# Kernel tuning notes

Hardware: AMD Instinct MI355X
Metric: run time of the kernel (lower is better)

## Reference

```python
import jax, jax.numpy as jnp
import numpy as np

B, C, L = 32, 512, 4096
H, K = 8, 3            # heads, kernel_size
D = C // H             # head dim
G = 32                 # GroupNorm groups
PAD = (K - 1) // 2
EPS = 1e-5
NEG = -1e30


def setup_inputs() -> dict:
    key = jax.random.key(0)
    ks = jax.random.split(key, 7)
    s = 0.02
    return {
        "x": jax.random.normal(ks[0], (B, C, L), dtype=jnp.float32),
        "gamma": jnp.ones((C,), dtype=jnp.float32),
        "beta": jnp.zeros((C,), dtype=jnp.float32),
        "W_k": jax.random.normal(ks[1], (C, H * D), dtype=jnp.float32) * s,
        "W_v": jax.random.normal(ks[2], (C, H * D), dtype=jnp.float32) * s,
        "W_o": jax.random.normal(ks[3], (H * D, C), dtype=jnp.float32) * s,
        "q": jax.random.normal(ks[4], (H, D), dtype=jnp.float32) * s,     # learned queries (QnA)
        "rpe": jax.random.normal(ks[5], (H, K), dtype=jnp.float32) * s,   # relative-position bias
    }


def _group_norm(x, gamma, beta):
    # x: (B, C, L); normalize over (C//G, L) within each of G groups
    b, c, l = x.shape
    xg = x.reshape(b, G, (c // G) * l)
    mu = jnp.mean(xg, axis=-1, keepdims=True)
    var = jnp.var(xg, axis=-1, keepdims=True)
    xn = ((xg - mu) * jax.lax.rsqrt(var + EPS)).reshape(b, c, l)
    return xn * gamma[None, :, None] + beta[None, :, None]


def reference(x, gamma, beta, W_k, W_v, W_o, q, rpe):
    h = _group_norm(x, gamma, beta)                     # (B, C, L)
    ht = jnp.transpose(h, (0, 2, 1))                    # (B, L, C)
    k = (ht @ W_k).reshape(B, L, H, D)                  # (B, L, H, D)
    v = (ht @ W_v).reshape(B, L, H, D)

    scale = 1.0 / np.sqrt(D).astype(np.float32)
    logits = jnp.einsum('blhd,hd->blh', k, q) * scale   # (B, L, H)

    # sliding windows of size K (zero-padded; -inf logits at boundaries)
    lp = jnp.pad(logits, ((0, 0), (PAD, PAD), (0, 0)), constant_values=NEG)
    lwin = jnp.stack([lp[:, j:j + L] for j in range(K)], axis=2)      # (B, L, K, H)
    lwin = lwin + jnp.transpose(rpe)[None, None]                       # rpe: (H,K)->(K,H)
    attn = jax.nn.softmax(lwin, axis=2)                                # (B, L, K, H)

    vp = jnp.pad(v, ((0, 0), (PAD, PAD), (0, 0), (0, 0)))
    vwin = jnp.stack([vp[:, j:j + L] for j in range(K)], axis=2)       # (B, L, K, H, D)
    o = jnp.einsum('blkh,blkhd->blhd', attn, vwin).reshape(B, L, H * D)

    out = (o @ W_o)                                      # (B, L, C)
    return x + jnp.transpose(out, (0, 2, 1))             # residual, (B, C, L)
```

## Files before the change

### kernel.cpp

```cpp
#include <hip/hip_runtime.h>

#define Bb 32
#define Cc 512
#define Ll 4096
#define Hh 8
#define Dd 64
#define Gg 32
#define BLt (Bb * Ll)
#define NKV 520
#define NKVPAD 640

typedef __attribute__((ext_vector_type(4))) float f32x4;
typedef __attribute__((ext_vector_type(8))) short short8;
typedef __attribute__((ext_vector_type(4))) short s16x4;
typedef __attribute__((ext_vector_type(4))) int int4v;

union U16 { int4v v; short s[8]; };

__device__ __forceinline__ float bf2f(short s) {
    unsigned u = ((unsigned)(unsigned short)s) << 16;
    float f; __builtin_memcpy(&f, &u, 4); return f;
}
__device__ __forceinline__ short f2bf(float f) {
    unsigned u; __builtin_memcpy(&u, &f, 4);
    u = (u + 0x7FFFu + ((u >> 16) & 1u)) >> 16;
    return (short)u;
}

__device__ __forceinline__ int kpack(int k) {
    int blk = k >> 5, r = k & 31;
    return blk * 32 + ((r & 15) >> 2) * 8 + ((r >> 4) << 2) + (r & 3);
}

__device__ __forceinline__ int swz_off(int row, int inner) {
    return row * 128 + (inner ^ ((row & 7) << 4));
}

__device__ __forceinline__ void gload16(const short* g, short* l) {
    __builtin_amdgcn_global_load_lds((const __attribute__((address_space(1))) unsigned int*)g,
                                     (__attribute__((address_space(3))) unsigned int*)l,
                                     16, 0, 0);
}

__global__ void k_prep(const float* __restrict__ Wk, const float* __restrict__ Wv,
                       const float* __restrict__ Wo, const float* __restrict__ q,
                       short* __restrict__ Wct, short* __restrict__ Wot, int packWo)
{
    int bid = blockIdx.x, t = threadIdx.x;
    if (bid < NKVPAD) {
        int n = bid;
        if (n < 512) {
            for (int k = t; k < 512; k += 64)
                Wct[n * 512 + kpack(k)] = f2bf(Wv[k * 512 + n]);
        } else if (n < NKV) {
            int h = n - 512;
            for (int k = t; k < 512; k += 64) {
                float acc = 0.f;
                for (int d = 0; d < 64; ++d)
                    acc += Wk[k * 512 + h * 64 + d] * q[h * 64 + d];
                Wct[n * 512 + kpack(k)] = f2bf(acc * 0.125f);
            }
        } else {
            for (int k = t; k < 512; k += 64) Wct[n * 512 + kpack(k)] = 0;
        }
    } else {
        int c = bid - NKVPAD;
        for (int k = t; k < 512; k += 64)
            Wot[c * 512 + (packWo ? kpack(k) : k)] = f2bf(Wo[k * 512 + c]);
    }
}

__global__ void k_stats(const float* __restrict__ x, float* __restrict__ stats)
{
    int bg = blockIdx.x;
    const float* p = x + (size_t)bg * 65536;
    int t = threadIdx.x;
    float s = 0.f, ss = 0.f;
    for (int i = t * 4; i < 65536; i += 1024) {
        f32x4 v = *(const f32x4*)(p + i);
        s  += v[0] + v[1] + v[2] + v[3];
        ss += v[0]*v[0] + v[1]*v[1] + v[2]*v[2] + v[3]*v[3];
    }
    for (int o = 32; o > 0; o >>= 1) { s += __shfl_down(s, o); ss += __shfl_down(ss, o); }
    __shared__ float red[8];
    int lane = t & 63, w = t >> 6;
    if (lane == 0) { red[w] = s; red[4 + w] = ss; }
    __syncthreads();
    if (t == 0) {
        float S  = red[0] + red[1] + red[2] + red[3];
        float SS = red[4] + red[5] + red[6] + red[7];
        float mean = S * (1.0f / 65536.0f);
        float var  = SS * (1.0f / 65536.0f) - mean * mean;
        stats[bg * 2]     = mean;
        stats[bg * 2 + 1] = rsqrtf(var + 1e-5f);
    }
}

__global__ void k_norm_t(const float* __restrict__ x, const float* __restrict__ gamma,
                         const float* __restrict__ beta, const float* __restrict__ stats,
                         short* __restrict__ hT)
{
    __shared__ float tile[64 * 65];
    int b = blockIdx.z, c0 = blockIdx.y * 64, l0 = blockIdx.x * 64;
    int t = threadIdx.x;
    int lq = t & 15, cq = t >> 4;
    #pragma unroll
    for (int p = 0; p < 4; ++p) {
        int cl = cq + p * 16;
        int c = c0 + cl;
        float mean = stats[(b * 32 + (c >> 4)) * 2];
        float rstd = stats[(b * 32 + (c >> 4)) * 2 + 1];
        float a  = rstd * gamma[c];
        float bb = beta[c] - mean * a;
        f32x4 v = *(const f32x4*)(x + ((size_t)b << 21) + ((size_t)c << 12) + l0 + lq * 4);
        #pragma unroll
        for (int j = 0; j < 4; ++j) tile[cl * 65 + lq * 4 + j] = v[j] * a + bb;
    }
    __syncthreads();
    int ll = t >> 2, cq4 = t & 3;
    int bl = b * Ll + l0 + ll;
    short hbuf[16];
    #pragma unroll
    for (int j = 0; j < 16; ++j) hbuf[j] = f2bf(tile[(cq4 * 16 + j) * 65 + ll]);
    short* dst = hT + (size_t)bl * 512 + ((c0 >> 5) + (cq4 >> 1)) * 32 + ((cq4 & 1) << 2);
    #pragma unroll
    for (int jj = 0; jj < 4; ++jj) {
        s16x4 v4 = { hbuf[jj*4+0], hbuf[jj*4+1], hbuf[jj*4+2], hbuf[jj*4+3] };
        *(s16x4*)(dst + jj * 8) = v4;
    }
}

template<bool PACKED>
__launch_bounds__(256, 2)
__global__ void k_gemm1(const short* __restrict__ A, const short* __restrict__ Bw,
                        short* __restrict__ vbuf, short* __restrict__ lbuf)
{
    __shared__ short sA[2][8192];
    __shared__ short sB[2][8192];
    const int t = threadIdx.x;
    const int m0 = blockIdx.y * 128;
    const int n0 = blockIdx.x * 128;
    const int lane = t & 63, wid = t >> 6;
    const int wm = wid >> 1, wn = wid & 1;
    const int g = lane >> 4, ln = lane & 15;

    const int srow = wid * 8 + (lane >> 3);
    const int sinner = (((lane & 7) ^ ((lane >> 3) & 7)) << 3);
    const short* gAs = A  + (size_t)(m0 + srow) * 512 + sinner;
    const short* gBs = Bw + (size_t)(n0 + srow) * 512 + sinner;

    f32x4 acc[4][4] = {};

    auto stage = [&](int kt, int buf) {
        #pragma unroll
        for (int gq = 0; gq < 4; ++gq) {
            gload16(gAs + (size_t)gq * 32 * 512 + kt * 64, &sA[buf][gq * 2048 + wid * 512]);
            gload16(gBs + (size_t)gq * 32 * 512 + kt * 64, &sB[buf][gq * 2048 + wid * 512]);
        }
    };
    auto compute = [&](int buf) {
        #pragma unroll
        for (int ks = 0; ks < 2; ++ks) {
            short8 af[4], bfr[4];
            #pragma unroll
            for (int i = 0; i < 4; ++i) {
                af[i]  = *(const short8*)((const char*)&sA[buf][0] + swz_off(wm * 64 + i * 16 + ln, ks * 64 + g * 16));
                bfr[i] = *(const short8*)((const char*)&sB[buf][0] + swz_off(wn * 64 + i * 16 + ln, ks * 64 + g * 16));
            }
            #pragma unroll
            for (int mi = 0; mi < 4; ++mi)
                #pragma unroll
                for (int ni = 0; ni < 4; ++ni)
                    acc[mi][ni] = __builtin_amdgcn_mfma_f32_16x16x32_bf16(af[mi], bfr[ni], acc[mi][ni], 0, 0, 0);
        }
    };

    stage(0, 0);
    __syncthreads();
    #pragma unroll 1
    for (int kt = 0; kt < 8; ++kt) {
        if (kt < 7) stage(kt + 1, (kt + 1) & 1);
        compute(kt & 1);
        __syncthreads();
    }

    #pragma unroll
    for (int mi = 0; mi < 4; ++mi)
        #pragma unroll
        for (int ni = 0; ni < 4; ++ni) {
            int n = n0 + wn * 64 + ni * 16 + ln;
            #pragma unroll
            for (int i = 0; i < 4; ++i) {
                int m = m0 + wm * 64 + mi * 16 + g * 4 + i;
                short val = f2bf(acc[mi][ni][i]);
                if constexpr (PACKED) {
                    if (n < 512)      vbuf[(size_t)m * 512 + kpack(n)] = val;
                    else if (n < NKV) lbuf[(size_t)m * 8 + (n - 512)] = val;
                } else {
                    if (n < NKV) vbuf[(size_t)m * NKV + n] = val;
                }
            }
        }
}

__global__ void k_combine(const short* __restrict__ vbuf, const short* __restrict__ lbuf,
                          const float* __restrict__ rpe, short* __restrict__ obuf)
{
    int t = threadIdx.x;
    int bl = blockIdx.x * 16 + (t >> 4);
    int blkd = t & 15;
    int h = blkd >> 1;
    int l = bl & (Ll - 1);
    int bm = (l == 0) ? bl : bl - 1;
    int bp = (l == Ll - 1) ? bl : bl + 1;
    float lg0 = (l > 0)      ? bf2f(lbuf[(size_t)bm * 8 + h]) + rpe[h * 3 + 0] : -1e30f;
    float lg1 =                bf2f(lbuf[(size_t)bl * 8 + h]) + rpe[h * 3 + 1];
    float lg2 = (l < Ll - 1) ? bf2f(lbuf[(size_t)bp * 8 + h]) + rpe[h * 3 + 2] : -1e30f;
    float m = fmaxf(lg1, fmaxf(lg0, lg2));
    float e0 = (l > 0)      ? __expf(lg0 - m) : 0.f;
    float e1 =                __expf(lg1 - m);
    float e2 = (l < Ll - 1) ? __expf(lg2 - m) : 0.f;
    float inv = 1.0f / (e0 + e1 + e2);
    float w0 = e0 * inv, w1 = e1 * inv, w2 = e2 * inv;

    const short8* vm = (const short8*)(vbuf + (size_t)bm * 512 + blkd * 32);
    const short8* v0 = (const short8*)(vbuf + (size_t)bl * 512 + blkd * 32);
    const short8* vp = (const short8*)(vbuf + (size_t)bp * 512 + blkd * 32);
    short8* dst = (short8*)(obuf + (size_t)bl * 512 + blkd * 32);
    #pragma unroll
    for (int qq = 0; qq < 4; ++qq) {
        short8 a = vm[qq], b = v0[qq], c = vp[qq], r;
        #pragma unroll
        for (int j = 0; j < 8; ++j)
            r[j] = f2bf(w0 * bf2f(a[j]) + w1 * bf2f(b[j]) + w2 * bf2f(c[j]));
        dst[qq] = r;
    }
}

__launch_bounds__(256, 2)
__global__ void k_gemm2p(const short* __restrict__ Wot, const short* __restrict__ obuf,
                         const float* __restrict__ x, float* __restrict__ out)
{
    __shared__ short sA[2][8192];
    __shared__ short sB[2][8192];
    const int t = threadIdx.x;
    const int m0 = blockIdx.x * 128;
    const int n0 = blockIdx.y * 128;
    const int lane = t & 63, wid = t >> 6;
    const int wm = wid >> 1, wn = wid & 1;
    const int g = lane >> 4, ln = lane & 15;

    const int srow = wid * 8 + (lane >> 3);
    const int sinner = (((lane & 7) ^ ((lane >> 3) & 7)) << 3);
    const short* gAs = Wot  + (size_t)(m0 + srow) * 512 + sinner;
    const short* gBs = obuf + (size_t)(n0 + srow) * 512 + sinner;

    f32x4 acc[4][4] = {};

    auto stage = [&](int kt, int buf) {
        #pragma unroll
        for (int gq = 0; gq < 4; ++gq) {
            gload16(gAs + (size_t)gq * 32 * 512 + kt * 64, &sA[buf][gq * 2048 + wid * 512]);
            gload16(gBs + (size_t)gq * 32 * 512 + kt * 64, &sB[buf][gq * 2048 + wid * 512]);
        }
    };
    auto compute = [&](int buf) {
        #pragma unroll
        for (int ks = 0; ks < 2; ++ks) {
            short8 af[4], bfr[4];
            #pragma unroll
            for (int i = 0; i < 4; ++i) {
                af[i]  = *(const short8*)((const char*)&sA[buf][0] + swz_off(wm * 64 + i * 16 + ln, ks * 64 + g * 16));
                bfr[i] = *(const short8*)((const char*)&sB[buf][0] + swz_off(wn * 64 + i * 16 + ln, ks * 64 + g * 16));
            }
            #pragma unroll
            for (int mi = 0; mi < 4; ++mi)
                #pragma unroll
                for (int ni = 0; ni < 4; ++ni)
                    acc[mi][ni] = __builtin_amdgcn_mfma_f32_16x16x32_bf16(af[mi], bfr[ni], acc[mi][ni], 0, 0, 0);
        }
    };

    stage(0, 0);
    __syncthreads();
    #pragma unroll 1
    for (int kt = 0; kt < 8; ++kt) {
        if (kt < 7) stage(kt + 1, (kt + 1) & 1);
        compute(kt & 1);
        __syncthreads();
    }

    #pragma unroll
    for (int mi = 0; mi < 4; ++mi)
        #pragma unroll
        for (int ni = 0; ni < 4; ++ni)
            #pragma unroll
            for (int i = 0; i < 4; ++i) {
                int c = m0 + wm * 64 + mi * 16 + g * 4 + i;
                int ng = n0 + wn * 64 + ni * 16 + ln;
                int b = ng >> 12, l = ng & (Ll - 1);
                size_t off = ((size_t)b << 21) | ((size_t)c << 12) | (size_t)l;
                out[off] = x[off] + acc[mi][ni][i];
            }
}

__global__ void k_attnw(const short* __restrict__ kv, const float* __restrict__ rpe,
                        float* __restrict__ attnW)
{
    int tid = blockIdx.x * 256 + threadIdx.x;
    int bl = tid >> 3, h = tid & 7;
    int l = bl & (Ll - 1);
    float lg[3];
    #pragma unroll
    for (int j = 0; j < 3; ++j) {
        bool valid = (j == 1) || (j == 0 && l > 0) || (j == 2 && l < Ll - 1);
        lg[j] = valid ? (bf2f(kv[(size_t)(bl + j - 1) * NKV + 512 + h]) + rpe[h * 3 + j])
                      : -1e30f;
    }
    float m = fmaxf(lg[0], fmaxf(lg[1], lg[2]));
    float e0 = __expf(lg[0] - m), e1 = __expf(lg[1] - m), e2 = __expf(lg[2] - m);
    float inv = 1.0f / (e0 + e1 + e2);
    f32x4 w = { e0 * inv, e1 * inv, e2 * inv, 0.0f };
    *(f32x4*)(attnW + (size_t)bl * 32 + h * 4) = w;
}

__launch_bounds__(256, 2)
__global__ void k_gemm2_fused(const short* __restrict__ Wot, const short* __restrict__ kv,
                              const float* __restrict__ attnW, const float* __restrict__ x,
                              float* __restrict__ out)
{
    __shared__ short sA[2][8192];
    __shared__ short sB[2][8192];
    const int t = threadIdx.x;
    const int m0 = blockIdx.x * 128;
    const int n0 = blockIdx.y * 128;
    const int lane = t & 63, wid = t >> 6;
    const int wm = wid >> 1, wn = wid & 1;
    const int g = lane >> 4, ln = lane & 15;
    const int sr = t >> 1, ksh = t & 1;

    const short* gA = Wot + (size_t)(m0 + sr) * 512 + ksh * 32;
    const int nrow = n0 + sr;
    const int lpos = nrow & (Ll - 1);
    const int nm1 = (lpos == 0) ? nrow : nrow - 1;
    const int np1 = (lpos == Ll - 1) ? nrow : nrow + 1;
    const short* gV0 = kv + (size_t)nrow * NKV + ksh * 32;
    const short* gVm = kv + (size_t)nm1  * NKV + ksh * 32;
    const short* gVp = kv + (size_t)np1  * NKV + ksh * 32;
    const float* gW = attnW + (size_t)nrow * 32;

    f32x4 acc[4][4] = {};
    U16 ra[4], rbm[4], rb0[4], rbp[4];
    f32x4 wv;

    auto load_tile = [&](int kt) {
        #pragma unroll
        for (int qq = 0; qq < 4; ++qq) {
            ra[qq].v  = *(const int4v*)(gA  + kt * 64 + qq * 8);
            rbm[qq].v = *(const int4v*)(gVm + kt * 64 + qq * 8);
            rb0[qq].v = *(const int4v*)(gV0 + kt * 64 + qq * 8);
            rbp[qq].v = *(const int4v*)(gVp + kt * 64 + qq * 8);
        }
        wv = *(const f32x4*)(gW + kt * 4);
    };
    auto write_tile = [&](int buf) {
        short ob[32];
        #pragma unroll
        for (int qq = 0; qq < 4; ++qq)
            #pragma unroll
            for (int j = 0; j < 8; ++j) {
                float o = wv[0] * bf2f(rbm[qq].s[j]) + wv[1] * bf2f(rb0[qq].s[j])
                        + wv[2] * bf2f(rbp[qq].s[j]);
                ob[qq * 8 + j] = f2bf(o);
            }
        #pragma unroll
        for (int f = 0; f < 4; ++f) {
            U16 wa, wb;
            #pragma unroll
            for (int j = 0; j < 4; ++j) {
                wa.s[j]     = ra[f >> 1].s[(f & 1) * 4 + j];
                wa.s[4 + j] = ra[2 + (f >> 1)].s[(f & 1) * 4 + j];
                wb.s[j]     = ob[4 * f + j];
                wb.s[4 + j] = ob[16 + 4 * f + j];
            }
            int off = swz_off(sr, ksh * 64 + f * 16);
            *(int4v*)((char*)&sA[buf][0] + off) = wa.v;
            *(int4v*)((char*)&sB[buf][0] + off) = wb.v;
        }
    };
    auto compute = [&](int buf) {
        #pragma unroll
        for (int ks = 0; ks < 2; ++ks) {
            short8 af[4], bfr[4];
            #pragma unroll
            for (int i = 0; i < 4; ++i) {
                af[i]  = *(const short8*)((const char*)&sA[buf][0] + swz_off(wm * 64 + i * 16 + ln, ks * 64 + g * 16));
                bfr[i] = *(const short8*)((const char*)&sB[buf][0] + swz_off(wn * 64 + i * 16 + ln, ks * 64 + g * 16));
            }
            #pragma unroll
            for (int mi = 0; mi < 4; ++mi)
                #pragma unroll
                for (int ni = 0; ni < 4; ++ni)
                    acc[mi][ni] = __builtin_amdgcn_mfma_f32_16x16x32_bf16(af[mi], bfr[ni], acc[mi][ni], 0, 0, 0);
        }
    };

    load_tile(0); write_tile(0); __syncthreads();
    #pragma unroll 1
    for (int kt = 0; kt < 8; ++kt) {
        if (kt < 7) load_tile(kt + 1);
        compute(kt & 1);
        if (kt < 7) write_tile((kt + 1) & 1);
        __syncthreads();
    }

    #pragma unroll
    for (int mi = 0; mi < 4; ++mi)
        #pragma unroll
        for (int ni = 0; ni < 4; ++ni)
            #pragma unroll
            for (int i = 0; i < 4; ++i) {
                int c = m0 + wm * 64 + mi * 16 + g * 4 + i;
                int ng = n0 + wn * 64 + ni * 16 + ln;
                int b = ng >> 12, l = ng & (Ll - 1);
                size_t off = ((size_t)b << 21) | ((size_t)c << 12) | (size_t)l;
                out[off] = x[off] + acc[mi][ni][i];
            }
}

extern "C" void kernel_launch(void* const* d_in, const int* in_sizes, int n_in,
                              void* d_out, int out_size, void* d_ws, size_t ws_size,
                              hipStream_t stream)
{
    const float* x     = (const float*)d_in[0];
    const float* gamma = (const float*)d_in[1];
    const float* beta  = (const float*)d_in[2];
    const float* Wk    = (const float*)d_in[3];
    const float* Wv    = (const float*)d_in[4];
    const float* Wo    = (const float*)d_in[5];
    const float* q     = (const float*)d_in[6];
    const float* rpe   = (const float*)d_in[7];
    float* out = (float*)d_out;
    char* ws = (char*)d_ws;

    const size_t MB128 = 134217728ull;
    const size_t MAIN_WS = MB128 * 2 + 655360 + 524288 + 2097152 + 8192;

    if (ws_size >= MAIN_WS) {
        short* obuf  = (short*)(ws);
        short* vbuf  = (short*)(ws + MB128);
        short* Wct   = (short*)(ws + 2 * MB128);
        short* Wot   = (short*)(ws + 2 * MB128 + 655360);
        short* lbuf  = (short*)(ws + 2 * MB128 + 655360 + 524288);
        float* stats = (float*)(ws + 2 * MB128 + 655360 + 524288 + 2097152);
        short* hT    = (short*)d_out;

        k_prep<<<1152, 64, 0, stream>>>(Wk, Wv, Wo, q, Wct, Wot, 1);
        k_stats<<<1024, 256, 0, stream>>>(x, stats);
        k_norm_t<<<dim3(64, 8, 32), 256, 0, stream>>>(x, gamma, beta, stats, hT);
        k_gemm1<true><<<dim3(5, 1024), 256, 0, stream>>>(hT, Wct, vbuf, lbuf);
        k_combine<<<8192, 256, 0, stream>>>(vbuf, lbuf, rpe, obuf);
        k_gemm2p<<<dim3(4, 1024), 256, 0, stream>>>(Wot, obuf, x, out);
    } else {
        short* Wct   = (short*)(ws + 0);
        short* Wot   = (short*)(ws + 655360);
        float* stats = (float*)(ws + 1179648);
        float* attnW = (float*)(ws + 1187840);
        short* kv    = (short*)(ws + 17965056);
        short* hT    = (short*)d_out;

        k_prep<<<1152, 64, 0, stream>>>(Wk, Wv, Wo, q, Wct, Wot, 0);
        k_stats<<<1024, 256, 0, stream>>>(x, stats);
        k_norm_t<<<dim3(64, 8, 32), 256, 0, stream>>>(x, gamma, beta, stats, hT);
        k_gemm1<false><<<dim3(5, 1024), 256, 0, stream>>>(hT, Wct, kv, nullptr);
        k_attnw<<<4096, 256, 0, stream>>>(kv, rpe, attnW);
        k_gemm2_fused<<<dim3(4, 1024), 256, 0, stream>>>(Wot, kv, attnW, x, out);
    }
}
```

Baseline: 575.1 us.

## Halve GEMM K-tile to raise occupancy and remap workgroups across XCDs

Both bf16 GEMM kernels now stage 32-wide K slices instead of 64, halving LDS use per block. The launch bound moves from 2 to 5 waves-per-EU, and the shared-memory swizzle is rewritten for 64-byte rows. Block IDs are also remapped so that consecutive tiles go to the same XCD, which should improve L2 reuse. The aim is more resident blocks to hide latency, at the cost of twice as many K iterations and barriers, and possible register pressure or spills under the tighter launch bound.

Result: slower. 682.0 us (+18.6%).

```diff
diff --git a/kernel.cpp b/kernel.cpp
--- a/kernel.cpp
+++ b/kernel.cpp
@@ -130,56 +130,59 @@
     }
 }
 
+
 template<bool PACKED>
-__launch_bounds__(256, 2)
+__launch_bounds__(256, 5)
 __global__ void k_gemm1(const short* __restrict__ A, const short* __restrict__ Bw,
                         short* __restrict__ vbuf, short* __restrict__ lbuf)
 {
-    __shared__ short sA[2][8192];
-    __shared__ short sB[2][8192];
+    __shared__ short sA[2][4096];
+    __shared__ short sB[2][4096];
     const int t = threadIdx.x;
-    const int m0 = blockIdx.y * 128;
-    const int n0 = blockIdx.x * 128;
+    const int nwg = gridDim.x * gridDim.y;
+    const int bid = blockIdx.x + gridDim.x * blockIdx.y;
+    const int work = (bid & 7) * (nwg >> 3) + (bid >> 3);
+    const int n0 = (work % gridDim.x) * 128;
+    const int m0 = (work / gridDim.x) * 128;
+
     const int lane = t & 63, wid = t >> 6;
     const int wm = wid >> 1, wn = wid & 1;
     const int g = lane >> 4, ln = lane & 15;
 
-    const int srow = wid * 8 + (lane >> 3);
-    const int sinner = (((lane & 7) ^ ((lane >> 3) & 7)) << 3);
-    const short* gAs = A  + (size_t)(m0 + srow) * 512 + sinner;
-    const short* gBs = Bw + (size_t)(n0 + srow) * 512 + sinner;
+    const int lrow = lane >> 2;
+    const int perm = (lane & 3) ^ ((lane >> 3) & 3);
+    const short* gA0 = A  + (size_t)(m0 + wid * 32 + lrow) * 512 + perm * 8;
+    const short* gB0 = Bw + (size_t)(n0 + wid * 32 + lrow) * 512 + perm * 8;
 
     f32x4 acc[4][4] = {};
 
     auto stage = [&](int kt, int buf) {
         #pragma unroll
-        for (int gq = 0; gq < 4; ++gq) {
-            gload16(gAs + (size_t)gq * 32 * 512 + kt * 64, &sA[buf][gq * 2048 + wid * 512]);
-            gload16(gBs + (size_t)gq * 32 * 512 + kt * 64, &sB[buf][gq * 2048 + wid * 512]);
+        for (int gq = 0; gq < 2; ++gq) {
+            gload16(gA0 + gq * 16 * 512 + kt * 32, &sA[buf][(wid * 2 + gq) * 512]);
+            gload16(gB0 + gq * 16 * 512 + kt * 32, &sB[buf][(wid * 2 + gq) * 512]);
         }
     };
     auto compute = [&](int buf) {
-        #pragma unroll
-        for (int ks = 0; ks < 2; ++ks) {
-            short8 af[4], bfr[4];
-            #pragma unroll
-            for (int i = 0; i < 4; ++i) {
-                af[i]  = *(const short8*)((const char*)&sA[buf][0] + swz_off(wm * 64 + i * 16 + ln, ks * 64 + g * 16));
-                bfr[i] = *(const short8*)((const char*)&sB[buf][0] + swz_off(wn * 64 + i * 16 + ln, ks * 64 + g * 16));
-            }
-            #pragma unroll
-            for (int mi = 0; mi < 4; ++mi)
-                #pragma unroll
-                for (int ni = 0; ni < 4; ++ni)
-                    acc[mi][ni] = __builtin_amdgcn_mfma_f32_16x16x32_bf16(af[mi], bfr[ni], acc[mi][ni], 0, 0, 0);
-        }
+        const int cc = g ^ ((ln >> 1) & 3);
+        short8 af[4], bfr[4];
+        #pragma unroll
+        for (int i = 0; i < 4; ++i) {
+            af[i]  = *(const short8*)((const char*)&sA[buf][0] + (wm * 64 + i * 16 + ln) * 64 + cc * 16);
+            bfr[i] = *(const short8*)((const char*)&sB[buf][0] + (wn * 64 + i * 16 + ln) * 64 + cc * 16);
+        }
+        #pragma unroll
+        for (int mi = 0; mi < 4; ++mi)
+            #pragma unroll
+            for (int ni = 0; ni < 4; ++ni)
+                acc[mi][ni] = __builtin_amdgcn_mfma_f32_16x16x32_bf16(af[mi], bfr[ni], acc[mi][ni], 0, 0, 0);
     };
 
     stage(0, 0);
     __syncthreads();
     #pragma unroll 1
-    for (int kt = 0; kt < 8; ++kt) {
-        if (kt < 7) stage(kt + 1, (kt + 1) & 1);
+    for (int kt = 0; kt < 16; ++kt) {
+        if (kt < 15) stage(kt + 1, (kt + 1) & 1);
         compute(kt & 1);
         __syncthreads();
     }
@@ -237,55 +240,57 @@
     }
 }
 
-__launch_bounds__(256, 2)
+__launch_bounds__(256, 5)
 __global__ void k_gemm2p(const short* __restrict__ Wot, const short* __restrict__ obuf,
                          const float* __restrict__ x, float* __restrict__ out)
 {
-    __shared__ short sA[2][8192];
-    __shared__ short sB[2][8192];
+    __shared__ short sA[2][4096];
+    __shared__ short sB[2][4096];
     const int t = threadIdx.x;
-    const int m0 = blockIdx.x * 128;
-    const int n0 = blockIdx.y * 128;
+    const int nwg = gridDim.x * gridDim.y;
+    const int bid = blockIdx.x + gridDim.x * blockIdx.y;
+    const int work = (bid & 7) * (nwg >> 3) + (bid >> 3);
+    const int m0 = (work % gridDim.x) * 128;
+    const int n0 = (work / gridDim.x) * 128;
+
     const int lane = t & 63, wid = t >> 6;
     const int wm = wid >> 1, wn = wid & 1;
     const int g = lane >> 4, ln = lane & 15;
 
-    const int srow = wid * 8 + (lane >> 3);
-    const int sinner = (((lane & 7) ^ ((lane >> 3) & 7)) << 3);
-    const short* gAs = Wot  + (size_t)(m0 + srow) * 512 + sinner;
-    const short* gBs = obuf + (size_t)(n0 + srow) * 512 + sinner;
+    const int lrow = lane >> 2;
+    const int perm = (lane & 3) ^ ((lane >> 3) & 3);
+    const short* gA0 = Wot  + (size_t)(m0 + wid * 32 + lrow) * 512 + perm * 8;
+    const short* gB0 = obuf + (size_t)(n0 + wid * 32 + lrow) * 512 + perm * 8;
 
     f32x4 acc[4][4] = {};
 
     auto stage = [&](int kt, int buf) {
         #pragma unroll
-        for (int gq = 0; gq < 4; ++gq) {
-            gload16(gAs + (size_t)gq * 32 * 512 + kt * 64, &sA[buf][gq * 2048 + wid * 512]);
-            gload16(gBs + (size_t)gq * 32 * 512 + kt * 64, &sB[buf][gq * 2048 + wid * 512]);
+        for (int gq = 0; gq < 2; ++gq) {
+            gload16(gA0 + gq * 16 * 512 + kt * 32, &sA[buf][(wid * 2 + gq) * 512]);
+            gload16(gB0 + gq * 16 * 512 + kt * 32, &sB[buf][(wid * 2 + gq) * 512]);
         }
     };
     auto compute = [&](int buf) {
-        #pragma unroll
-        for (int ks = 0; ks < 2; ++ks) {
-            short8 af[4], bfr[4];
-            #pragma unroll
-            for (int i = 0; i < 4; ++i) {
-                af[i]  = *(const short8*)((const char*)&sA[buf][0] + swz_off(wm * 64 + i * 16 + ln, ks * 64 + g * 16));
-                bfr[i] = *(const short8*)((const char*)&sB[buf][0] + swz_off(wn * 64 + i * 16 + ln, ks * 64 + g * 16));
-            }
-            #pragma unroll
-            for (int mi = 0; mi < 4; ++mi)
-                #pragma unroll
-                for (int ni = 0; ni < 4; ++ni)
-                    acc[mi][ni] = __builtin_amdgcn_mfma_f32_16x16x32_bf16(af[mi], bfr[ni], acc[mi][ni], 0, 0, 0);
-        }
+        const int cc = g ^ ((ln >> 1) & 3);
+        short8 af[4], bfr[4];
+        #pragma unroll
+        for (int i = 0; i < 4; ++i) {
+            af[i]  = *(const short8*)((const char*)&sA[buf][0] + (wm * 64 + i * 16 + ln) * 64 + cc * 16);
+            bfr[i] = *(const short8*)((const char*)&sB[buf][0] + (wn * 64 + i * 16 + ln) * 64 + cc * 16);
+        }
+        #pragma unroll
+        for (int mi = 0; mi < 4; ++mi)
+            #pragma unroll
+            for (int ni = 0; ni < 4; ++ni)
+                acc[mi][ni] = __builtin_amdgcn_mfma_f32_16x16x32_bf16(af[mi], bfr[ni], acc[mi][ni], 0, 0, 0);
     };
 
     stage(0, 0);
     __syncthreads();
     #pragma unroll 1
-    for (int kt = 0; kt < 8; ++kt) {
-        if (kt < 7) stage(kt + 1, (kt + 1) & 1);
+    for (int kt = 0; kt < 16; ++kt) {
+        if (kt < 15) stage(kt + 1, (kt + 1) & 1);
         compute(kt & 1);
         __syncthreads();
     }
```

## Deepen GEMM prefetch with vmcnt waits, XCD-aware block remap, LDS-staged vector stores

Applied to the files above, without the earlier changes.

Both GEMM kernels now issue two K-tiles of async global-to-LDS loads up front. Each iteration waits with explicit s_waitcnt vmcnt and raw barriers instead of __syncthreads, so the load for tile k+2 overlaps compute on tile k. Block IDs are remapped so consecutive tiles land on the same XCD, which should improve L2 reuse. The packed gemm1 epilogue stages bf16 results through LDS and writes 16-byte vector stores instead of scattered 2-byte stores. The price is hand-written wait counts that depend on exact load counts and fragile scheduling fences.

New measurement: 542.4 us. -5.7%, faster.

```diff
diff --git a/kernel.cpp b/kernel.cpp
--- a/kernel.cpp
+++ b/kernel.cpp
@@ -41,6 +41,9 @@
                                      (__attribute__((address_space(3))) unsigned int*)l,
                                      16, 0, 0);
 }
+
+#define BAR() __builtin_amdgcn_s_barrier()
+#define SFENCE() __builtin_amdgcn_sched_barrier(0)
 
 __global__ void k_prep(const float* __restrict__ Wk, const float* __restrict__ Wv,
                        const float* __restrict__ Wo, const float* __restrict__ q,
@@ -130,6 +133,7 @@
     }
 }
 
+
 template<bool PACKED>
 __launch_bounds__(256, 2)
 __global__ void k_gemm1(const short* __restrict__ A, const short* __restrict__ Bw,
@@ -138,8 +142,12 @@
     __shared__ short sA[2][8192];
     __shared__ short sB[2][8192];
     const int t = threadIdx.x;
-    const int m0 = blockIdx.y * 128;
-    const int n0 = blockIdx.x * 128;
+    const int nwg = gridDim.x * gridDim.y;
+    const int bid = blockIdx.x + gridDim.x * blockIdx.y;
+    const int work = (bid & 7) * (nwg >> 3) + (bid >> 3);
+    const int n0 = (work % gridDim.x) * 128;
+    const int m0 = (work / gridDim.x) * 128;
+
     const int lane = t & 63, wid = t >> 6;
     const int wm = wid >> 1, wn = wid & 1;
     const int g = lane >> 4, ln = lane & 15;
@@ -175,32 +183,73 @@
         }
     };
 
-    stage(0, 0);
-    __syncthreads();
+    stage(0, 0); stage(1, 1);
     #pragma unroll 1
     for (int kt = 0; kt < 8; ++kt) {
-        if (kt < 7) stage(kt + 1, (kt + 1) & 1);
+        if (kt < 7) asm volatile("s_waitcnt vmcnt(8)" ::: "memory");
+        else        asm volatile("s_waitcnt vmcnt(0)" ::: "memory");
+        BAR(); SFENCE();
         compute(kt & 1);
-        __syncthreads();
-    }
-
-    #pragma unroll
-    for (int mi = 0; mi < 4; ++mi)
-        #pragma unroll
-        for (int ni = 0; ni < 4; ++ni) {
-            int n = n0 + wn * 64 + ni * 16 + ln;
-            #pragma unroll
-            for (int i = 0; i < 4; ++i) {
-                int m = m0 + wm * 64 + mi * 16 + g * 4 + i;
-                short val = f2bf(acc[mi][ni][i]);
-                if constexpr (PACKED) {
-                    if (n < 512)      vbuf[(size_t)m * 512 + kpack(n)] = val;
-                    else if (n < NKV) lbuf[(size_t)m * 8 + (n - 512)] = val;
-                } else {
-                    if (n < NKV) vbuf[(size_t)m * NKV + n] = val;
+        SFENCE();
+        if (kt < 6) { BAR(); stage(kt + 2, kt & 1); }
+    }
+
+    if constexpr (PACKED) {
+        if (n0 < 512) {
+            BAR();
+            short* scr = &sA[0][0] + wid * 4096;
+            #pragma unroll
+            for (int mi = 0; mi < 4; ++mi)
+                #pragma unroll
+                for (int ni = 0; ni < 4; ++ni)
+                    #pragma unroll
+                    for (int i = 0; i < 4; ++i)
+                        scr[(mi * 16 + g * 4 + i) * 64 + ni * 16 + ln] = f2bf(acc[mi][ni][i]);
+            asm volatile("s_waitcnt lgkmcnt(0)" ::: "memory");
+            SFENCE();
+            const int c8 = lane & 7, blkq = c8 >> 2, jq = c8 & 3;
+            #pragma unroll
+            for (int it = 0; it < 8; ++it) {
+                int mrow = it * 8 + (lane >> 3);
+                const short* bp = scr + mrow * 64 + blkq * 32;
+                s16x4 lo = *(const s16x4*)(bp + 4 * jq);
+                s16x4 hi = *(const s16x4*)(bp + 16 + 4 * jq);
+                union { int4v v; s16x4 h[2]; } ov;
+                ov.h[0] = lo; ov.h[1] = hi;
+                int m = m0 + wm * 64 + mrow;
+                int nc = n0 + wn * 64 + blkq * 32 + jq * 8;
+                *(int4v*)(vbuf + (size_t)m * 512 + nc) = ov.v;
+            }
+        } else {
+            #pragma unroll
+            for (int mi = 0; mi < 4; ++mi)
+                #pragma unroll
+                for (int ni = 0; ni < 4; ++ni) {
+                    int n = n0 + wn * 64 + ni * 16 + ln;
+                    if (n >= 512 && n < NKV) {
+                        #pragma unroll
+                        for (int i = 0; i < 4; ++i) {
+                            int m = m0 + wm * 64 + mi * 16 + g * 4 + i;
+                            lbuf[(size_t)m * 8 + (n - 512)] = f2bf(acc[mi][ni][i]);
+                        }
+                    }
                 }
-            }
-        }
+        }
+    } else {
+        #pragma unroll
+        for (int mi = 0; mi < 4; ++mi)
+            #pragma unroll
+            for (int ni = 0; ni < 4; ++ni) {
+                int n = n0 + wn * 64 + ni * 16 + ln;
+                if (n < NKV) {
+                    #pragma unroll
+                    for (int i = 0; i < 4; ++i) {
+                        int m = m0 + wm * 64 + mi * 16 + g * 4 + i;
+                        vbuf[(size_t)m * NKV + n] = f2bf(acc[mi][ni][i]);
+                    }
+                }
+            }
+    }
 }
 
 __global__ void k_combine(const short* __restrict__ vbuf, const short* __restrict__ lbuf,
@@ -244,8 +293,12 @@
     __shared__ short sA[2][8192];
     __shared__ short sB[2][8192];
     const int t = threadIdx.x;
-    const int m0 = blockIdx.x * 128;
-    const int n0 = blockIdx.y * 128;
+    const int nwg = gridDim.x * gridDim.y;
+    const int bid = blockIdx.x + gridDim.x * blockIdx.y;
+    const int work = (bid & 7) * (nwg >> 3) + (bid >> 3);
+    const int m0 = (work % gridDim.x) * 128;
+    const int n0 = (work / gridDim.x) * 128;
+
     const int lane = t & 63, wid = t >> 6;
     const int wm = wid >> 1, wn = wid & 1;
     const int g = lane >> 4, ln = lane & 15;
@@ -281,13 +334,15 @@
         }
     };
 
-    stage(0, 0);
-    __syncthreads();
+    stage(0, 0); stage(1, 1);
     #pragma unroll 1
     for (int kt = 0; kt < 8; ++kt) {
-        if (kt < 7) stage(kt + 1, (kt + 1) & 1);
+        if (kt < 7) asm volatile("s_waitcnt vmcnt(8)" ::: "memory");
+        else        asm volatile("s_waitcnt vmcnt(0)" ::: "memory");
+        BAR(); SFENCE();
         compute(kt & 1);
-        __syncthreads();
+        SFENCE();
+        if (kt < 6) { BAR(); stage(kt + 2, kt & 1); }
     }
 
     #pragma unroll
```
